# Kernel tuning notes

Hardware: AMD Instinct MI355X
Metric: run time of the kernel (lower is better)

The kernel has to match this reference:

```python
import jax, jax.numpy as jnp
import numpy as np
from jax import lax

SCALE = 128.0        # x/y/w/h scale = model input size
MIN_SCORE = 0.5      # min_score_thresh
IOU_THRESH = 0.3     # mediapipe min_suppression_threshold
MAX_DET = 64         # fixed detection slots (jit-safe replacement for dynamic list)
NUM_ANCHORS = 896


def _decode(raw_boxes, anchors):
    # raw_boxes [B,A,16], anchors [A,4] = (x_center, y_center, w, h)
    ax, ay, aw, ah = anchors[:, 0], anchors[:, 1], anchors[:, 2], anchors[:, 3]
    xc = raw_boxes[..., 0] / SCALE * aw + ax
    yc = raw_boxes[..., 1] / SCALE * ah + ay
    w = raw_boxes[..., 2] / SCALE * aw
    h = raw_boxes[..., 3] / SCALE * ah
    box = jnp.stack([yc - h / 2, xc - w / 2, yc + h / 2, xc + w / 2], axis=-1)  # [B,A,4] ymin,xmin,ymax,xmax
    kp = raw_boxes[..., 4:16].reshape(*raw_boxes.shape[:-1], 6, 2)  # [B,A,6,2] (x,y)
    kpx = kp[..., 0] / SCALE * aw[:, None] + ax[:, None]
    kpy = kp[..., 1] / SCALE * ah[:, None] + ay[:, None]
    kps = jnp.stack([kpx, kpy], axis=-1).reshape(*raw_boxes.shape[:-1], 12)
    return jnp.concatenate([box, kps], axis=-1)  # [B,A,16]


def _iou(box, boxes):
    # box [4], boxes [A,4]; coords = ymin,xmin,ymax,xmax
    ymin = jnp.maximum(box[0], boxes[:, 0])
    xmin = jnp.maximum(box[1], boxes[:, 1])
    ymax = jnp.minimum(box[2], boxes[:, 2])
    xmax = jnp.minimum(box[3], boxes[:, 3])
    inter = jnp.maximum(ymax - ymin, 0.0) * jnp.maximum(xmax - xmin, 0.0)
    a1 = jnp.maximum(box[2] - box[0], 0.0) * jnp.maximum(box[3] - box[1], 0.0)
    a2 = jnp.maximum(boxes[:, 2] - boxes[:, 0], 0.0) * jnp.maximum(boxes[:, 3] - boxes[:, 1], 0.0)
    return inter / jnp.maximum(a1 + a2 - inter, 1e-6)


def _weighted_nms_single(coords, scores):
    # coords [A,16], scores [A] -> out [MAX_DET,17] sorted by descending score, zero-padded
    rem = jnp.where(scores >= MIN_SCORE, scores, -1.0)

    def step(rem, _):
        idx = jnp.argmax(rem)
        best = rem[idx]
        iou = _iou(coords[idx, :4], coords[:, :4])
        overlap = (iou > IOU_THRESH) & (rem > 0.0)
        wts = jnp.where(overlap, scores, 0.0)            # weight = candidate score
        denom = jnp.maximum(wts.sum(), 1e-6)
        blended = (coords * wts[:, None]).sum(0) / denom  # weighted box + keypoints
        det = jnp.concatenate([blended, best[None]])
        det = jnp.where(best > 0.0, det, jnp.zeros(17, det.dtype))
        rem = jnp.where(overlap, -1.0, rem)
        return rem, det

    _, out = lax.scan(step, rem, None, length=MAX_DET)
    return out


def _project(dets, matrix):
    # dets [B,MAX_DET,17], matrix [B,8] (first two rows of row-major 4x4 affine)
    m = matrix[:, None, :]  # [B,1,8]
    x_idx = jnp.array([1, 3, 4, 6, 8, 10, 12, 14])
    y_idx = jnp.array([0, 2, 5, 7, 9, 11, 13, 15])
    xs = dets[..., x_idx]
    ys = dets[..., y_idx]
    new_x = xs * m[..., 0:1] + ys * m[..., 1:2] + m[..., 3:4]
    new_y = xs * m[..., 4:5] + ys * m[..., 5:6] + m[..., 7:8]
    out = dets.at[..., x_idx].set(new_x)
    out = out.at[..., y_idx].set(new_y)
    # keep padded (invalid) rows zero, like the segmented-tensor original
    valid = dets[..., 16:17] > 0.0
    return jnp.where(valid, out, 0.0)


def _rescale(dets, h, w):
    hf = jnp.float32(h)
    wf = jnp.float32(w)
    scale = jnp.concatenate([
        jnp.array([1.0, 1.0]) * 0 + jnp.stack([hf, wf]),   # ymin*h, xmin*w
        jnp.stack([hf, wf]),                               # ymax*h, xmax*w
        jnp.tile(jnp.stack([wf, hf]), 6),                  # kp x*w, kp y*h
        jnp.ones((1,), jnp.float32),                       # score unchanged
    ])
    return dets * scale


def setup_inputs() -> dict:
    key = jax.random.key(0)
    k1, k2, k3, k4 = jax.random.split(key, 4)
    B = 2048
    return {
        "raw_boxes": jax.random.normal(k1, (B, NUM_ANCHORS, 16), jnp.float32),
        "raw_scores": jax.random.normal(k2, (B, NUM_ANCHORS), jnp.float32),
        "anchors": jax.random.uniform(k3, (NUM_ANCHORS, 4), jnp.float32),
        "transform_matrix": jax.random.normal(k4, (B, 8), jnp.float32),
        "h": 720,
        "w": 1280,
    }


def reference(raw_boxes, raw_scores, anchors, transform_matrix, h, w):
    coords = _decode(raw_boxes, anchors)                       # [B,A,16]
    scores = jax.nn.sigmoid(jnp.clip(raw_scores, -100.0, 100.0))
    dets = jax.vmap(_weighted_nms_single)(coords, scores)      # [B,MAX_DET,17]
    dets = _project(dets, transform_matrix)
    dets = _rescale(dets, h, w)
    return dets
```

## Files before the change

kernel.cpp:

```cpp
#include <hip/hip_runtime.h>
#include <math.h>

#define NANCH 896
#define MAXD 64
#define NS 14

template <int NSLOT>
__device__ __forceinline__ void nms_loop(
    const int lane, const int nact,
    const float4* __restrict__ cbox, const float* __restrict__ cscore,
    const unsigned short* __restrict__ cidx, float* __restrict__ sdet,
    const float* __restrict__ rb, const float* __restrict__ anchors,
    const float m0, const float m1, const float m3,
    const float m4, const float m5, const float m7,
    const float hf, const float wf, float* __restrict__ ob)
{
    const float inv = 1.f / 128.f;

    float cb0[NSLOT], cb1[NSLOT], cb2[NSLOT], cb3[NSLOT], car[NSLOT], rem[NSLOT];
    int   corig[NSLOT];
#pragma unroll
    for (int k = 0; k < NSLOT; ++k) {
        int p = k * 64 + lane;
        bool v = (p < nact);
        int pc = v ? p : 0;
        float4 bb = cbox[pc];
        cb0[k] = bb.x; cb1[k] = bb.y; cb2[k] = bb.z; cb3[k] = bb.w;
        car[k] = fmaxf(bb.z - bb.x, 0.f) * fmaxf(bb.w - bb.y, 0.f);
        corig[k] = (int)cidx[pc];
        rem[k] = v ? cscore[pc] : -1.f;
    }

    const bool isx = (lane < 16) && ((0x555Au >> lane) & 1u);

    int iter = 0;
    while (true) {
        float bv = -2.f; int bi = 1 << 30;
#pragma unroll
        for (int j = 0; j < NSLOT; ++j) {
            if (rem[j] > bv) { bv = rem[j]; bi = j * 64 + lane; }
        }
#pragma unroll
        for (int s2 = 32; s2 >= 1; s2 >>= 1) {
            float ov = __shfl_xor(bv, s2, 64);
            int   oi = __shfl_xor(bi, s2, 64);
            if (ov > bv || (ov == bv && oi < bi)) { bv = ov; bi = oi; }
        }

        if (bv <= 0.f) {
            int n = (MAXD - iter) * 17;
            float* op = ob + iter * 17;
            for (int e = lane; e < n; e += 64) op[e] = 0.f;
            break;
        }

        float4 bb = cbox[bi];
        const float bby0 = bb.x, bbx0 = bb.y, bby1 = bb.z, bbx1 = bb.w;
        const float a1 = fmaxf(bby1 - bby0, 0.f) * fmaxf(bbx1 - bbx0, 0.f);

        float acc[16];
#pragma unroll
        for (int c = 0; c < 16; ++c) acc[c] = 0.f;
        float wsum = 0.f;
        bool anyov = false;

#pragma unroll
        for (int j = 0; j < NSLOT; ++j) {
            float yA = fmaxf(bby0, cb0[j]);
            float xA = fmaxf(bbx0, cb1[j]);
            float yB = fminf(bby1, cb2[j]);
            float xB = fminf(bbx1, cb3[j]);
            float inter = fmaxf(yB - yA, 0.f) * fmaxf(xB - xA, 0.f);
            if (inter > 0.f) {
                float iou = inter / fmaxf(a1 + car[j] - inter, 1e-6f);
                if (iou > 0.3f && rem[j] > 0.f) {
                    anyov = true;
                    float wj = rem[j];
                    rem[j] = -1.f;
                    wsum += wj;
                    acc[0] += cb0[j] * wj; acc[1] += cb1[j] * wj;
                    acc[2] += cb2[j] * wj; acc[3] += cb3[j] * wj;
                    const int orig = corig[j];
                    float4 an = *(const float4*)(anchors + orig * 4);
                    const float* rp = rb + orig * 16;
                    float4 r1 = *(const float4*)(rp + 4);
                    float4 r2 = *(const float4*)(rp + 8);
                    float4 r3 = *(const float4*)(rp + 12);
                    acc[4]  += (r1.x * inv * an.z + an.x) * wj;
                    acc[5]  += (r1.y * inv * an.w + an.y) * wj;
                    acc[6]  += (r1.z * inv * an.z + an.x) * wj;
                    acc[7]  += (r1.w * inv * an.w + an.y) * wj;
                    acc[8]  += (r2.x * inv * an.z + an.x) * wj;
                    acc[9]  += (r2.y * inv * an.w + an.y) * wj;
                    acc[10] += (r2.z * inv * an.z + an.x) * wj;
                    acc[11] += (r2.w * inv * an.w + an.y) * wj;
                    acc[12] += (r3.x * inv * an.z + an.x) * wj;
                    acc[13] += (r3.y * inv * an.w + an.y) * wj;
                    acc[14] += (r3.z * inv * an.z + an.x) * wj;
                    acc[15] += (r3.w * inv * an.w + an.y) * wj;
                }
            }
        }

        const unsigned long long mm = __ballot(anyov);
        const bool stuck = (mm == 0ull);

        float q, dnm;
        if (stuck) {
            q = 0.f; dnm = 1e-6f;
        } else if (__popcll(mm) == 1) {
            const int src = (int)__ffsll((long long)mm) - 1;
            float t = __shfl(acc[0], src, 64);
#pragma unroll
            for (int c = 1; c < 16; ++c) {
                float tc = __shfl(acc[c], src, 64);
                t = (lane == c) ? tc : t;
            }
            q   = t;
            dnm = fmaxf(__shfl(wsum, src, 64), 1e-6f);
        } else {
#pragma unroll
            for (int s2 = 32; s2 >= 1; s2 >>= 1) {
                wsum += __shfl_xor(wsum, s2, 64);
#pragma unroll
                for (int c = 0; c < 16; ++c) acc[c] += __shfl_xor(acc[c], s2, 64);
            }
            float t = acc[0];
#pragma unroll
            for (int c2 = 1; c2 < 16; ++c2) t = (lane == c2) ? acc[c2] : t;
            q = t; dnm = fmaxf(wsum, 1e-6f);
        }

        q = q / dnm;
        const float p = __shfl(q, lane ^ 1, 64);
        const float detc = (lane >= 16) ? bv
                         : (isx ? (q * m0 + p * m1 + m3) * wf
                                : (p * m4 + q * m5 + m7) * hf);

        if (stuck) {
            if (lane < 17) sdet[lane] = detc;
            int n = (MAXD - iter) * 17;
            float* op = ob + iter * 17;
            int c = lane % 17;
            for (int e = lane; e < n; e += 64) {
                op[e] = sdet[c];
                c += 13; if (c >= 17) c -= 17;
            }
            break;
        } else {
            if (lane < 17) ob[iter * 17 + lane] = detc;
            ++iter;
            if (iter == MAXD) break;
        }
    }
}

__global__ __launch_bounds__(64, 2) void blaze_wave_kernel(
    const float* __restrict__ raw_boxes,
    const float* __restrict__ raw_scores,
    const float* __restrict__ anchors,
    const float* __restrict__ tmat,
    const int* __restrict__ hptr,
    const int* __restrict__ wptr,
    float* __restrict__ out,
    int B)
{
    __shared__ float4 cbox[NANCH];
    __shared__ float  cscore[NANCH];
    __shared__ unsigned short cidx[NANCH];
    __shared__ float  sdet[17];

    const int lane = threadIdx.x;
    const int b    = blockIdx.x;
    if (b >= B) return;

    const float* rb = raw_boxes  + (size_t)b * (NANCH * 16);
    const float* rs = raw_scores + (size_t)b * NANCH;
    const float inv = 1.f / 128.f;

    const float* M = tmat + (size_t)b * 8;
    const float m0 = M[0], m1 = M[1], m3 = M[3];
    const float m4 = M[4], m5 = M[5], m7 = M[7];
    const float hf = (float)(*hptr);
    const float wf = (float)(*wptr);

    float xv[NS];
#pragma unroll
    for (int j = 0; j < NS; ++j) xv[j] = rs[lane + 64 * j];

    bool  act[NS];
    float4 r0v[NS], anv[NS];
#pragma unroll
    for (int j = 0; j < NS; ++j) {
        act[j] = (xv[j] >= 0.f);
        const int a2 = act[j] ? (lane + 64 * j) : 0;
        r0v[j] = *(const float4*)(rb + a2 * 16);
        anv[j] = *(const float4*)(anchors + a2 * 4);
    }

    float sv[NS];
#pragma unroll
    for (int j = 0; j < NS; ++j) {
        float x = fminf(fmaxf(xv[j], -100.f), 100.f);
        sv[j] = 1.f / (1.f + expf(-x));
    }

    int base = 0;
#pragma unroll
    for (int j = 0; j < NS; ++j) {
        float xc = r0v[j].x * inv * anv[j].z + anv[j].x;
        float yc = r0v[j].y * inv * anv[j].w + anv[j].y;
        float ww = r0v[j].z * inv * anv[j].z;
        float hh = r0v[j].w * inv * anv[j].w;
        float y0 = yc - hh * 0.5f, x0 = xc - ww * 0.5f;
        float y1 = yc + hh * 0.5f, x1 = xc + ww * 0.5f;
        unsigned long long m = __ballot(act[j]);
        int pos = base + __popcll(m & ((1ull << lane) - 1ull));
        if (act[j]) {
            cbox[pos]   = make_float4(y0, x0, y1, x1);
            cscore[pos] = sv[j];
            cidx[pos]   = (unsigned short)(lane + 64 * j);
        }
        base += __popcll(m);
    }
    const int nact = base;
    const int nsc  = (nact + 63) >> 6;

    float* ob = out + (size_t)b * (MAXD * 17);

    if (nsc <= 7)
        nms_loop<7>(lane, nact, cbox, cscore, cidx, sdet, rb, anchors,
                    m0, m1, m3, m4, m5, m7, hf, wf, ob);
    else if (nsc <= 8)
        nms_loop<8>(lane, nact, cbox, cscore, cidx, sdet, rb, anchors,
                    m0, m1, m3, m4, m5, m7, hf, wf, ob);
    else if (nsc <= 10)
        nms_loop<10>(lane, nact, cbox, cscore, cidx, sdet, rb, anchors,
                     m0, m1, m3, m4, m5, m7, hf, wf, ob);
    else
        nms_loop<14>(lane, nact, cbox, cscore, cidx, sdet, rb, anchors,
                     m0, m1, m3, m4, m5, m7, hf, wf, ob);
}

extern "C" void kernel_launch(void* const* d_in, const int* in_sizes, int n_in,
                              void* d_out, int out_size, void* d_ws, size_t ws_size,
                              hipStream_t stream) {
    (void)n_in; (void)out_size; (void)d_ws; (void)ws_size;
    const float* raw_boxes  = (const float*)d_in[0];
    const float* raw_scores = (const float*)d_in[1];
    const float* anchors    = (const float*)d_in[2];
    const float* tmat       = (const float*)d_in[3];
    const int*   hptr       = (const int*)d_in[4];
    const int*   wptr       = (const int*)d_in[5];
    float* out = (float*)d_out;

    const int B = in_sizes[0] / (NANCH * 16);
    blaze_wave_kernel<<<B, 64, 0, stream>>>(raw_boxes, raw_scores, anchors,
                                            tmat, hptr, wptr, out, B);
}
```

Baseline: 186.0 us.

## Defer detection projection and output writes to a batched epilogue via LDS row buffer

The NMS loop no longer projects and stores each detection as it is found. Instead, one lane writes the raw accumulated sums, score and weight sum for each detection into a shared-memory row buffer, and a separate epilogue loop later normalises, projects and writes all 64 output rows, including the stuck-mode replication and zero padding. The intent is to shorten the serial per-iteration critical path by removing the shuffle-based lane selection, the divide and the global store from the loop. The row buffer reuses the shared memory of the score and index arrays, which are only read before the loop, and the change adds LDS traffic and an extra pass over the output.

```diff
diff --git a/kernel.cpp b/kernel.cpp
--- a/kernel.cpp
+++ b/kernel.cpp
@@ -9,7 +9,7 @@
 __device__ __forceinline__ void nms_loop(
     const int lane, const int nact,
     const float4* __restrict__ cbox, const float* __restrict__ cscore,
-    const unsigned short* __restrict__ cidx, float* __restrict__ sdet,
+    const unsigned short* __restrict__ cidx, float* __restrict__ rowbuf,
     const float* __restrict__ rb, const float* __restrict__ anchors,
     const float m0, const float m1, const float m3,
     const float m4, const float m5, const float m7,
@@ -31,8 +31,7 @@
         rem[k] = v ? cscore[pc] : -1.f;
     }
 
-    const bool isx = (lane < 16) && ((0x555Au >> lane) & 1u);
-
+    int nrows; bool stuckmode = false;
     int iter = 0;
     while (true) {
         float bv = -2.f; int bi = 1 << 30;
@@ -47,12 +46,7 @@
             if (ov > bv || (ov == bv && oi < bi)) { bv = ov; bi = oi; }
         }
 
-        if (bv <= 0.f) {
-            int n = (MAXD - iter) * 17;
-            float* op = ob + iter * 17;
-            for (int e = lane; e < n; e += 64) op[e] = 0.f;
-            break;
-        }
+        if (bv <= 0.f) { nrows = iter; break; }
 
         float4 bb = cbox[bi];
         const float bby0 = bb.x, bbx0 = bb.y, bby1 = bb.z, bbx1 = bb.w;
@@ -103,21 +97,27 @@
         }
 
         const unsigned long long mm = __ballot(anyov);
-        const bool stuck = (mm == 0ull);
-
-        float q, dnm;
-        if (stuck) {
-            q = 0.f; dnm = 1e-6f;
-        } else if (__popcll(mm) == 1) {
+        float* rowp = rowbuf + iter * 20;
+
+        if (mm == 0ull) {
+            if (lane == 0) {
+                *(float4*)(rowp +  0) = make_float4(0.f, 0.f, 0.f, 0.f);
+                *(float4*)(rowp +  4) = make_float4(0.f, 0.f, 0.f, 0.f);
+                *(float4*)(rowp +  8) = make_float4(0.f, 0.f, 0.f, 0.f);
+                *(float4*)(rowp + 12) = make_float4(0.f, 0.f, 0.f, 0.f);
+                rowp[16] = bv; rowp[17] = 0.f;
+            }
+            nrows = iter; stuckmode = true; break;
+        }
+        if (__popcll(mm) == 1) {
             const int src = (int)__ffsll((long long)mm) - 1;
-            float t = __shfl(acc[0], src, 64);
-#pragma unroll
-            for (int c = 1; c < 16; ++c) {
-                float tc = __shfl(acc[c], src, 64);
-                t = (lane == c) ? tc : t;
-            }
-            q   = t;
-            dnm = fmaxf(__shfl(wsum, src, 64), 1e-6f);
+            if (lane == src) {
+                *(float4*)(rowp +  0) = make_float4(acc[0],  acc[1],  acc[2],  acc[3]);
+                *(float4*)(rowp +  4) = make_float4(acc[4],  acc[5],  acc[6],  acc[7]);
+                *(float4*)(rowp +  8) = make_float4(acc[8],  acc[9],  acc[10], acc[11]);
+                *(float4*)(rowp + 12) = make_float4(acc[12], acc[13], acc[14], acc[15]);
+                rowp[16] = bv; rowp[17] = wsum;
+            }
         } else {
 #pragma unroll
             for (int s2 = 32; s2 >= 1; s2 >>= 1) {
@@ -125,33 +125,36 @@
 #pragma unroll
                 for (int c = 0; c < 16; ++c) acc[c] += __shfl_xor(acc[c], s2, 64);
             }
-            float t = acc[0];
-#pragma unroll
-            for (int c2 = 1; c2 < 16; ++c2) t = (lane == c2) ? acc[c2] : t;
-            q = t; dnm = fmaxf(wsum, 1e-6f);
-        }
-
-        q = q / dnm;
-        const float p = __shfl(q, lane ^ 1, 64);
-        const float detc = (lane >= 16) ? bv
-                         : (isx ? (q * m0 + p * m1 + m3) * wf
-                                : (p * m4 + q * m5 + m7) * hf);
-
-        if (stuck) {
-            if (lane < 17) sdet[lane] = detc;
-            int n = (MAXD - iter) * 17;
-            float* op = ob + iter * 17;
-            int c = lane % 17;
-            for (int e = lane; e < n; e += 64) {
-                op[e] = sdet[c];
-                c += 13; if (c >= 17) c -= 17;
-            }
-            break;
-        } else {
-            if (lane < 17) ob[iter * 17 + lane] = detc;
-            ++iter;
-            if (iter == MAXD) break;
-        }
+            if (lane == 0) {
+                *(float4*)(rowp +  0) = make_float4(acc[0],  acc[1],  acc[2],  acc[3]);
+                *(float4*)(rowp +  4) = make_float4(acc[4],  acc[5],  acc[6],  acc[7]);
+                *(float4*)(rowp +  8) = make_float4(acc[8],  acc[9],  acc[10], acc[11]);
+                *(float4*)(rowp + 12) = make_float4(acc[12], acc[13], acc[14], acc[15]);
+                rowp[16] = bv; rowp[17] = wsum;
+            }
+        }
+        ++iter;
+        if (iter == MAXD) { nrows = MAXD; break; }
+    }
+
+    const bool isx = (lane < 16) && ((0x555Au >> lane) & 1u);
+#pragma unroll 4
+    for (int r = 0; r < MAXD; ++r) {
+        const int sr = (r < nrows) ? r : (stuckmode ? nrows : -1);
+        float detc = 0.f;
+        if (sr >= 0) {
+            const float* rowp = rowbuf + sr * 20;
+            const float tv  = rowp[lane & 15];
+            const float scv = rowp[16];
+            const float wsv = rowp[17];
+            const float dnm = fmaxf(wsv, 1e-6f);
+            float q = tv / dnm;
+            const float p = __shfl(q, lane ^ 1, 64);
+            detc = (lane >= 16) ? scv
+                 : (isx ? (q * m0 + p * m1 + m3) * wf
+                        : (p * m4 + q * m5 + m7) * hf);
+        }
+        if (lane < 17) ob[r * 17 + lane] = detc;
     }
 }
 
@@ -166,9 +169,10 @@
     int B)
 {
     __shared__ float4 cbox[NANCH];
-    __shared__ float  cscore[NANCH];
-    __shared__ unsigned short cidx[NANCH];
-    __shared__ float  sdet[17];
+    __shared__ __align__(16) unsigned char upool[5376];
+    float*          cscore = (float*)upool;
+    unsigned short* cidx   = (unsigned short*)(upool + 3584);
+    float*          rowbuf = (float*)upool;
 
     const int lane = threadIdx.x;
     const int b    = blockIdx.x;
@@ -229,16 +233,16 @@
     float* ob = out + (size_t)b * (MAXD * 17);
 
     if (nsc <= 7)
-        nms_loop<7>(lane, nact, cbox, cscore, cidx, sdet, rb, anchors,
+        nms_loop<7>(lane, nact, cbox, cscore, cidx, rowbuf, rb, anchors,
                     m0, m1, m3, m4, m5, m7, hf, wf, ob);
     else if (nsc <= 8)
-        nms_loop<8>(lane, nact, cbox, cscore, cidx, sdet, rb, anchors,
+        nms_loop<8>(lane, nact, cbox, cscore, cidx, rowbuf, rb, anchors,
                     m0, m1, m3, m4, m5, m7, hf, wf, ob);
     else if (nsc <= 10)
-        nms_loop<10>(lane, nact, cbox, cscore, cidx, sdet, rb, anchors,
+        nms_loop<10>(lane, nact, cbox, cscore, cidx, rowbuf, rb, anchors,
                      m0, m1, m3, m4, m5, m7, hf, wf, ob);
     else
-        nms_loop<14>(lane, nact, cbox, cscore, cidx, sdet, rb, anchors,
+        nms_loop<14>(lane, nact, cbox, cscore, cidx, rowbuf, rb, anchors,
                      m0, m1, m3, m4, m5, m7, hf, wf, ob);
 }
 
```

New measurement: 196.1 us. 1.05x slower.

## Pre-sort candidates with wave bitonic sort to replace per-iteration argmax

Applied to the files above, without the earlier changes.

For batches with at most 512 active candidates, the candidates are first bitonic-sorted in registers by a packed (score, index) 64-bit key, using in-register swaps across slots and cross-lane shuffles. Each NMS iteration then picks the next surviving candidate with a ballot over the sorted order, replacing the full argmax reduction. Broadcasts of the chosen box and of single-lane accumulators use readlane instead of shuffles. The cost is an upfront sort of about 8 slots with many 64-bit shuffle stages, and a fixed 8-slot register footprint even for the smaller cases that previously used 7 slots.

```diff
diff --git a/kernel.cpp b/kernel.cpp
--- a/kernel.cpp
+++ b/kernel.cpp
@@ -4,6 +4,214 @@
 #define NANCH 896
 #define MAXD 64
 #define NS 14
+
+#define SLOTSTAGE(JS, K)                                                     \
+    {                                                                        \
+        _Pragma("unroll")                                                    \
+        for (int s = 0; s < 8; ++s) if ((s & (JS)) == 0) {                   \
+            const int s2 = s | (JS);                                         \
+            const bool up = (((s << 6) & (K)) == 0);                         \
+            unsigned long long a = ik[s], b = ik[s2];                        \
+            unsigned long long mn = (a < b) ? a : b;                         \
+            unsigned long long mx = (a < b) ? b : a;                         \
+            ik[s] = up ? mn : mx; ik[s2] = up ? mx : mn;                     \
+        }                                                                    \
+    }
+
+__device__ __forceinline__ float rdlane(float v, int sl) {
+    return __uint_as_float((unsigned)__builtin_amdgcn_readlane(__float_as_int(v), sl));
+}
+
+__device__ __forceinline__ void sorted_nms(
+    const int lane, const int nact,
+    const float4* __restrict__ cbox, const float* __restrict__ cscore,
+    const unsigned short* __restrict__ cidx, float* __restrict__ sdet,
+    const float* __restrict__ rb, const float* __restrict__ anchors,
+    const float m0, const float m1, const float m3,
+    const float m4, const float m5, const float m7,
+    const float hf, const float wf, float* __restrict__ ob)
+{
+    const float inv = 1.f / 128.f;
+
+    unsigned long long ik[8];
+#pragma unroll
+    for (int s = 0; s < 8; ++s) {
+        const int p = s * 64 + lane;
+        unsigned long long key = 0ull;
+        if (p < nact) {
+            key = ((unsigned long long)__float_as_uint(cscore[p]) << 10)
+                | (unsigned long long)(1023 - p);
+        }
+        ik[s] = ~key;
+    }
+
+    for (int k = 2; k <= 512; k <<= 1) {
+        if (k == 128)      { SLOTSTAGE(1, 128) }
+        else if (k == 256) { SLOTSTAGE(2, 256) SLOTSTAGE(1, 256) }
+        else if (k == 512) { SLOTSTAGE(4, 512) SLOTSTAGE(2, 512) SLOTSTAGE(1, 512) }
+        const int jstart = ((k >> 1) > 32) ? 32 : (k >> 1);
+        for (int j = jstart; j > 0; j >>= 1) {
+#pragma unroll
+            for (int s = 0; s < 8; ++s) {
+                unsigned long long a = ik[s];
+                unsigned plo = (unsigned)__shfl_xor((int)(unsigned)a, j, 64);
+                unsigned phi = (unsigned)__shfl_xor((int)(unsigned)(a >> 32), j, 64);
+                unsigned long long b = ((unsigned long long)phi << 32) | plo;
+                const bool up    = ((((s << 6) | lane) & k) == 0);
+                const bool lower = ((lane & j) == 0);
+                unsigned long long mn = (a < b) ? a : b;
+                unsigned long long mx = (a < b) ? b : a;
+                ik[s] = ((up == lower) ? mn : mx);
+            }
+        }
+    }
+
+    unsigned long long skey[8];
+    float sb0[8], sb1[8], sb2[8], sb3[8], sar[8], sw[8];
+    int sorig[8];
+#pragma unroll
+    for (int s = 0; s < 8; ++s) {
+        const unsigned long long key = ~ik[s];
+        skey[s] = key;
+        const int pc = (key != 0ull) ? (1023 - (int)(key & 1023ull)) : 0;
+        float4 bb = cbox[pc];
+        sb0[s] = bb.x; sb1[s] = bb.y; sb2[s] = bb.z; sb3[s] = bb.w;
+        sar[s] = fmaxf(bb.z - bb.x, 0.f) * fmaxf(bb.w - bb.y, 0.f);
+        sorig[s] = (int)cidx[pc];
+        sw[s] = __uint_as_float((unsigned)(key >> 10));
+    }
+
+    const bool isx = (lane < 16) && ((0x555Au >> lane) & 1u);
+
+    int cur = 0, iter = 0;
+    while (true) {
+        unsigned am = 0;
+#pragma unroll
+        for (int s = 0; s < 8; ++s) am |= (skey[s] != 0ull) ? (1u << s) : 0u;
+        unsigned long long m = 0ull;
+        while (cur < 8) {
+            m = __ballot(((am >> cur) & 1u) != 0u);
+            if (m != 0ull) break;
+            ++cur;
+        }
+        if (m == 0ull) {
+            int n = (MAXD - iter) * 17;
+            float* op = ob + iter * 17;
+            for (int e = lane; e < n; e += 64) op[e] = 0.f;
+            break;
+        }
+        const int bl = (int)__ffsll((long long)m) - 1;
+
+        float o0 = sb0[0], o1 = sb1[0], o2 = sb2[0], o3 = sb3[0],
+              oa = sar[0], os = sw[0];
+#pragma unroll
+        for (int s = 1; s < 8; ++s) {
+            const bool c = (cur == s);
+            o0 = c ? sb0[s] : o0; o1 = c ? sb1[s] : o1;
+            o2 = c ? sb2[s] : o2; o3 = c ? sb3[s] : o3;
+            oa = c ? sar[s] : oa; os = c ? sw[s]  : os;
+        }
+        const float bby0 = rdlane(o0, bl), bbx0 = rdlane(o1, bl);
+        const float bby1 = rdlane(o2, bl), bbx1 = rdlane(o3, bl);
+        const float a1   = rdlane(oa, bl);
+        const float bv   = rdlane(os, bl);
+
+        float acc[16];
+#pragma unroll
+        for (int c = 0; c < 16; ++c) acc[c] = 0.f;
+        float wsum = 0.f;
+        bool anyov = false;
+
+#pragma unroll
+        for (int j = 0; j < 8; ++j) {
+            float yA = fmaxf(bby0, sb0[j]);
+            float xA = fmaxf(bbx0, sb1[j]);
+            float yB = fminf(bby1, sb2[j]);
+            float xB = fminf(bbx1, sb3[j]);
+            float inter = fmaxf(yB - yA, 0.f) * fmaxf(xB - xA, 0.f);
+            if (inter > 0.f) {
+                float iou = inter / fmaxf(a1 + sar[j] - inter, 1e-6f);
+                if (iou > 0.3f && skey[j] != 0ull) {
+                    anyov = true;
+                    const float wj = sw[j];
+                    skey[j] = 0ull;
+                    wsum += wj;
+                    acc[0] += sb0[j] * wj; acc[1] += sb1[j] * wj;
+                    acc[2] += sb2[j] * wj; acc[3] += sb3[j] * wj;
+                    const int orig = sorig[j];
+                    float4 an = *(const float4*)(anchors + orig * 4);
+                    const float* rp = rb + orig * 16;
+                    float4 r1 = *(const float4*)(rp + 4);
+                    float4 r2 = *(const float4*)(rp + 8);
+                    float4 r3 = *(const float4*)(rp + 12);
+                    acc[4]  += (r1.x * inv * an.z + an.x) * wj;
+                    acc[5]  += (r1.y * inv * an.w + an.y) * wj;
+                    acc[6]  += (r1.z * inv * an.z + an.x) * wj;
+                    acc[7]  += (r1.w * inv * an.w + an.y) * wj;
+                    acc[8]  += (r2.x * inv * an.z + an.x) * wj;
+                    acc[9]  += (r2.y * inv * an.w + an.y) * wj;
+                    acc[10] += (r2.z * inv * an.z + an.x) * wj;
+                    acc[11] += (r2.w * inv * an.w + an.y) * wj;
+                    acc[12] += (r3.x * inv * an.z + an.x) * wj;
+                    acc[13] += (r3.y * inv * an.w + an.y) * wj;
+                    acc[14] += (r3.z * inv * an.z + an.x) * wj;
+                    acc[15] += (r3.w * inv * an.w + an.y) * wj;
+                }
+            }
+        }
+
+        const unsigned long long mm = __ballot(anyov);
+        const bool stuck = (mm == 0ull);
+
+        float q, dnm;
+        if (stuck) {
+            q = 0.f; dnm = 1e-6f;
+        } else if (__popcll(mm) == 1) {
+            const int src = (int)__ffsll((long long)mm) - 1;
+            float t = rdlane(acc[0], src);
+#pragma unroll
+            for (int c = 1; c < 16; ++c) {
+                const float tc = rdlane(acc[c], src);
+                t = (lane == c) ? tc : t;
+            }
+            q   = t;
+            dnm = fmaxf(rdlane(wsum, src), 1e-6f);
+        } else {
+#pragma unroll
+            for (int s2 = 32; s2 >= 1; s2 >>= 1) {
+                wsum += __shfl_xor(wsum, s2, 64);
+#pragma unroll
+                for (int c = 0; c < 16; ++c) acc[c] += __shfl_xor(acc[c], s2, 64);
+            }
+            float t = acc[0];
+#pragma unroll
+            for (int c2 = 1; c2 < 16; ++c2) t = (lane == c2) ? acc[c2] : t;
+            q = t; dnm = fmaxf(wsum, 1e-6f);
+        }
+
+        q = q / dnm;
+        const float p = __shfl(q, lane ^ 1, 64);
+        const float detc = (lane >= 16) ? bv
+                         : (isx ? (q * m0 + p * m1 + m3) * wf
+                                : (p * m4 + q * m5 + m7) * hf);
+
+        if (stuck) {
+            if (lane < 17) sdet[lane] = detc;
+            int n = (MAXD - iter) * 17;
+            float* op = ob + iter * 17;
+            int c = lane % 17;
+            for (int e = lane; e < n; e += 64) {
+                op[e] = sdet[c];
+                c += 13; if (c >= 17) c -= 17;
+            }
+            break;
+        } else {
+            if (lane < 17) ob[iter * 17 + lane] = detc;
+            ++iter;
+            if (iter == MAXD) break;
+        }
+    }
+}
 
 template <int NSLOT>
 __device__ __forceinline__ void nms_loop(
@@ -16,7 +224,6 @@
     const float hf, const float wf, float* __restrict__ ob)
 {
     const float inv = 1.f / 128.f;
-
     float cb0[NSLOT], cb1[NSLOT], cb2[NSLOT], cb3[NSLOT], car[NSLOT], rem[NSLOT];
     int   corig[NSLOT];
 #pragma unroll
@@ -30,9 +237,7 @@
         corig[k] = (int)cidx[pc];
         rem[k] = v ? cscore[pc] : -1.f;
     }
-
     const bool isx = (lane < 16) && ((0x555Au >> lane) & 1u);
-
     int iter = 0;
     while (true) {
         float bv = -2.f; int bi = 1 << 30;
@@ -46,24 +251,20 @@
             int   oi = __shfl_xor(bi, s2, 64);
             if (ov > bv || (ov == bv && oi < bi)) { bv = ov; bi = oi; }
         }
-
         if (bv <= 0.f) {
             int n = (MAXD - iter) * 17;
             float* op = ob + iter * 17;
             for (int e = lane; e < n; e += 64) op[e] = 0.f;
             break;
         }
-
         float4 bb = cbox[bi];
         const float bby0 = bb.x, bbx0 = bb.y, bby1 = bb.z, bbx1 = bb.w;
         const float a1 = fmaxf(bby1 - bby0, 0.f) * fmaxf(bbx1 - bbx0, 0.f);
-
         float acc[16];
 #pragma unroll
         for (int c = 0; c < 16; ++c) acc[c] = 0.f;
         float wsum = 0.f;
         bool anyov = false;
-
 #pragma unroll
         for (int j = 0; j < NSLOT; ++j) {
             float yA = fmaxf(bby0, cb0[j]);
@@ -101,10 +302,8 @@
                 }
             }
         }
-
         const unsigned long long mm = __ballot(anyov);
         const bool stuck = (mm == 0ull);
-
         float q, dnm;
         if (stuck) {
             q = 0.f; dnm = 1e-6f;
@@ -130,13 +329,11 @@
             for (int c2 = 1; c2 < 16; ++c2) t = (lane == c2) ? acc[c2] : t;
             q = t; dnm = fmaxf(wsum, 1e-6f);
         }
-
         q = q / dnm;
         const float p = __shfl(q, lane ^ 1, 64);
         const float detc = (lane >= 16) ? bv
                          : (isx ? (q * m0 + p * m1 + m3) * wf
                                 : (p * m4 + q * m5 + m7) * hf);
-
         if (stuck) {
             if (lane < 17) sdet[lane] = detc;
             int n = (MAXD - iter) * 17;
@@ -228,12 +425,9 @@
 
     float* ob = out + (size_t)b * (MAXD * 17);
 
-    if (nsc <= 7)
-        nms_loop<7>(lane, nact, cbox, cscore, cidx, sdet, rb, anchors,
-                    m0, m1, m3, m4, m5, m7, hf, wf, ob);
-    else if (nsc <= 8)
-        nms_loop<8>(lane, nact, cbox, cscore, cidx, sdet, rb, anchors,
-                    m0, m1, m3, m4, m5, m7, hf, wf, ob);
+    if (nsc <= 8)
+        sorted_nms(lane, nact, cbox, cscore, cidx, sdet, rb, anchors,
+                   m0, m1, m3, m4, m5, m7, hf, wf, ob);
     else if (nsc <= 10)
         nms_loop<10>(lane, nact, cbox, cscore, cidx, sdet, rb, anchors,
                      m0, m1, m3, m4, m5, m7, hf, wf, ob);
```

After: 206.0 us. 10.8% more time.
